# Optimization experiments

Hardware: AMD Instinct MI355X
Metric: run time of the kernel (lower is better)

Reference implementation:

```python
import jax, jax.numpy as jnp
import numpy as np

D = 512
H = 4
DK = D // H
N_ACTOR = 4096
N_BV = 4096
NEG = jnp.float32(-1e9)  # stands in for -inf; exp underflows to exactly 0 in fp32


def setup_inputs() -> dict:
    key = jax.random.key(0)
    k1, k2, k3, k4, k5, k6, k7, k8 = jax.random.split(key, 8)
    a_z = jax.random.normal(k1, (N_ACTOR, D), dtype=jnp.float32)
    bv_z = jax.random.normal(k2, (N_BV, D), dtype=jnp.float32)
    mask = jax.random.uniform(k3, (N_ACTOR, N_BV)) > 0.5
    weight = jax.random.normal(k4, (N_ACTOR, N_BV), dtype=jnp.float32)
    # nn.MultiheadAttention parameters (packed in_proj, out_proj)
    in_proj_w = jax.random.normal(k5, (3 * D, D), dtype=jnp.float32) * 0.02
    in_proj_b = jax.random.normal(k6, (3 * D,), dtype=jnp.float32) * 0.02
    out_w = jax.random.normal(k7, (D, D), dtype=jnp.float32) * 0.02
    out_b = jax.random.normal(k8, (D,), dtype=jnp.float32) * 0.02
    return {"a_z": a_z, "bv_z": bv_z, "mask": mask, "weight": weight,
            "in_proj_w": in_proj_w, "in_proj_b": in_proj_b,
            "out_w": out_w, "out_b": out_b}


def reference(a_z, bv_z, mask, weight, in_proj_w, in_proj_b, out_w, out_b):
    n, d = a_z.shape
    m = bv_z.shape[0]
    a = jnp.nan_to_num(a_z, nan=0.0, posinf=1.0, neginf=-1.0)
    kv = jnp.nan_to_num(bv_z, nan=0.0, posinf=1.0, neginf=-1.0)
    w = jnp.nan_to_num(weight, nan=0.0, posinf=1.0, neginf=-1.0)
    mf = mask.astype(a.dtype)
    valid = jnp.any(mask, axis=1)  # actors with at least one unmasked key

    # attn_mask = weight masked with -inf at padded keys (covers key_padding_mask too)
    bias = jnp.where(mask, w, NEG)  # [n, m]

    wq, wk, wv = jnp.split(in_proj_w, 3, axis=0)
    bq, bk, bv = jnp.split(in_proj_b, 3, axis=0)
    q = ((a @ wq.T + bq).reshape(n, H, DK)) * (1.0 / np.sqrt(DK))
    k = (kv @ wk.T + bk).reshape(m, H, DK)
    v = (kv @ wv.T + bv).reshape(m, H, DK)

    scores = jnp.einsum('nhd,mhd->nhm', q, k) + bias[:, None, :]
    attn = jax.nn.softmax(scores, axis=-1)                  # [n, h, m]
    ctx = jnp.einsum('nhm,mhd->nhd', attn, v).reshape(n, d)
    out = ctx @ out_w.T + out_b                              # out_proj

    # topic alignment: mean over head-chunks of the projected output
    topic = out.reshape(n, H, DK).mean(axis=1)               # [n, dk]

    # influence: softmax-normalized weight scores dotted with avg attn weights
    aw = attn.mean(axis=1) * mf                              # head-averaged attn, masked
    norm_scores = jax.nn.softmax(bias, axis=-1) * mf
    influence = jnp.sum(norm_scores * aw, axis=-1)           # [n]

    # actors with no valid key are scattered back as zeros
    topic = jnp.where(valid[:, None], topic, 0.0)
    influence = jnp.where(valid, influence, 0.0)
    return topic, influence
```

## Files before the change

kernel.cpp:

```cpp
#include <hip/hip_runtime.h>
#include <hip/hip_bf16.h>
#include <cstdint>
#include <cstddef>


typedef __attribute__((ext_vector_type(8))) short bf16x8;
typedef __attribute__((ext_vector_type(4))) short bf16x4;
typedef __attribute__((ext_vector_type(4))) float f32x4;

#define MFMA32(a, b, c) __builtin_amdgcn_mfma_f32_16x16x32_bf16((a), (b), (c), 0, 0, 0)
#define MFMA16(a, b, c) __builtin_amdgcn_mfma_f32_16x16x16bf16_1k((a), (b), (c), 0, 0, 0)

static __device__ __forceinline__ short f2b(float x) {
  union { float f; unsigned u; } v; v.f = x;
  unsigned r = v.u + 0x7fffu + ((v.u >> 16) & 1u);
  return (short)(r >> 16);
}

__global__ __launch_bounds__(256) void k_qkv(
    const float* __restrict__ a, const float* __restrict__ kv,
    const float* __restrict__ w, const float* __restrict__ bias,
    short* __restrict__ Qb, short* __restrict__ Kp, short* __restrict__ Vp)
{
  __shared__ short As[128 * 40];
  __shared__ short Bs[128 * 40];
  const int blk = blockIdx.x;
  const int bm = blk / 12, bn = blk % 12;
  const int m0 = bm * 128, n0 = bn * 128;
  const float* __restrict__ Ain = (bn < 4) ? a : kv;
  const int tid = threadIdx.x;
  const int lane = tid & 63, wv = tid >> 6;
  const int wm = (wv >> 1) * 64, wn = (wv & 1) * 64;
  const int c = lane & 15, g = lane >> 4;
  const int srow = tid >> 1, scol = (tid & 1) * 16;

  f32x4 acc[4][4];
#pragma unroll
  for (int i = 0; i < 4; ++i)
#pragma unroll
    for (int j = 0; j < 4; ++j) acc[i][j] = (f32x4)0.f;

  for (int k0 = 0; k0 < 512; k0 += 32) {
    const float* ap = Ain + (size_t)(m0 + srow) * 512 + k0 + scol;
    const float* bp = w + (size_t)(n0 + srow) * 512 + k0 + scol;
#pragma unroll
    for (int j = 0; j < 4; ++j) {
      f32x4 av = *(const f32x4*)(ap + 4 * j);
      f32x4 bv = *(const f32x4*)(bp + 4 * j);
      bf16x4 as, bs;
      as.x = f2b(av.x); as.y = f2b(av.y); as.z = f2b(av.z); as.w = f2b(av.w);
      bs.x = f2b(bv.x); bs.y = f2b(bv.y); bs.z = f2b(bv.z); bs.w = f2b(bv.w);
      *(bf16x4*)(&As[srow * 40 + scol + 4 * j]) = as;
      *(bf16x4*)(&Bs[srow * 40 + scol + 4 * j]) = bs;
    }
    __syncthreads();
    bf16x8 af[4], bfg[4];
#pragma unroll
    for (int t = 0; t < 4; ++t) {
      af[t]  = *(const bf16x8*)(&As[(wm + t * 16 + c) * 40 + g * 8]);
      bfg[t] = *(const bf16x8*)(&Bs[(wn + t * 16 + c) * 40 + g * 8]);
    }
#pragma unroll
    for (int rt = 0; rt < 4; ++rt)
#pragma unroll
      for (int ct = 0; ct < 4; ++ct)
        acc[rt][ct] = MFMA32(af[rt], bfg[ct], acc[rt][ct]);
    __syncthreads();
  }

#pragma unroll
  for (int ct = 0; ct < 4; ++ct) {
    const int col = n0 + wn + ct * 16 + c;
    const float bj = bias[col];
#pragma unroll
    for (int rt = 0; rt < 4; ++rt) {
      const int row = m0 + wm + rt * 16 + g * 4;
      const int mc = row >> 4;
      if (bn < 4) {
#pragma unroll
        for (int r = 0; r < 4; ++r)
          Qb[(size_t)(row + r) * 512 + col] = f2b((acc[rt][ct][r] + bj) * 0.08838834764831843f);
      } else if (bn < 8) {
        const int colK = col - 512;
        const int h = colK >> 7, dk = colK & 127;
        const int ks = dk >> 5, gk = (dk >> 3) & 3, j = dk & 7;
        short* base = Kp + (size_t)((((h * 256 + mc) * 4 + ks) * 64) + gk * 16 + g * 4) * 8 + j;
#pragma unroll
        for (int r = 0; r < 4; ++r) base[r * 8] = f2b(acc[rt][ct][r] + bj);
      } else {
        const int colV = col - 1024;
        const int h = colV >> 7, db = (colV & 127) >> 4, cv = colV & 15;
        bf16x4 pk;
#pragma unroll
        for (int r = 0; r < 4; ++r) pk[r] = f2b(acc[rt][ct][r] + bj);
        *(bf16x4*)(Vp + (size_t)((((h * 256 + mc) * 8 + db) * 64) + g * 16 + cv) * 4) = pk;
      }
    }
  }
}

__global__ __launch_bounds__(256, 4) void k_attn(
    const short* __restrict__ Qb, const short* __restrict__ Kp,
    const short* __restrict__ Vp, const float* __restrict__ wgt,
    const int* __restrict__ msk, const int S,
    short* __restrict__ Opart, float* __restrict__ lpart,
    float* __restrict__ cipart, float* __restrict__ lbpart)
{
  const int bx = blockIdx.x;
  const int rb = bx & 255, sp = bx >> 8;
  const int n0 = rb * 16;
  const int mlen = 4096 / S;
  const int mc0 = (sp * mlen) >> 4;
  const int nch = mlen >> 4;
  const int tid = threadIdx.x;
  const int lane = tid & 63, h = tid >> 6;
  const int c = lane & 15, g = lane >> 4;

  bf16x8 qf[4];
#pragma unroll
  for (int ks = 0; ks < 4; ++ks)
    qf[ks] = *(const bf16x8*)(Qb + (size_t)(n0 + c) * 512 + h * 128 + ks * 32 + g * 8);

  f32x4 O[8];
#pragma unroll
  for (int db = 0; db < 8; ++db) O[db] = (f32x4)0.f;
  float lh = 0.f, lb = 0.f, ci = 0.f;

  const short* Kw = Kp + (size_t)h * 524288 + (size_t)lane * 8;
  const short* Vw = Vp + (size_t)h * 524288 + (size_t)lane * 4;
  const size_t ebase = (size_t)(n0 + c) * 4096 + g * 4;

  for (int t = 0; t < nch; ++t) {
    const int mc = mc0 + t;
    const int4 mk = *(const int4*)(msk + ebase + mc * 16);
    const f32x4 wvv = *(const f32x4*)(wgt + ebase + mc * 16);
    bf16x8 kf[4];
#pragma unroll
    for (int ks = 0; ks < 4; ++ks)
      kf[ks] = *(const bf16x8*)(Kw + mc * 2048 + ks * 512);
    f32x4 Sv = (f32x4)0.f;
#pragma unroll
    for (int ks = 0; ks < 4; ++ks) Sv = MFMA32(kf[ks], qf[ks], Sv);
    const float e0 = mk.x ? __expf(wvv.x) : 0.f;
    const float e1 = mk.y ? __expf(wvv.y) : 0.f;
    const float e2 = mk.z ? __expf(wvv.z) : 0.f;
    const float e3 = mk.w ? __expf(wvv.w) : 0.f;
    const float p0 = __expf(Sv[0]) * e0, p1 = __expf(Sv[1]) * e1;
    const float p2 = __expf(Sv[2]) * e2, p3 = __expf(Sv[3]) * e3;
    lh += (p0 + p1) + (p2 + p3);
    lb += (e0 + e1) + (e2 + e3);
    ci += (p0 * e0 + p1 * e1) + (p2 * e2 + p3 * e3);
    bf16x4 pa;
    pa[0] = f2b(p0); pa[1] = f2b(p1); pa[2] = f2b(p2); pa[3] = f2b(p3);
#pragma unroll
    for (int db = 0; db < 8; ++db) {
      const bf16x4 vf = *(const bf16x4*)(Vw + mc * 2048 + db * 256);
      O[db] = MFMA16(pa, vf, O[db]);
    }
  }

  lh += __shfl_xor(lh, 16, 64); lh += __shfl_xor(lh, 32, 64);
  lb += __shfl_xor(lb, 16, 64); lb += __shfl_xor(lb, 32, 64);
  ci += __shfl_xor(ci, 16, 64); ci += __shfl_xor(ci, 32, 64);

  float inv[4];
#pragma unroll
  for (int r = 0; r < 4; ++r)
    inv[r] = 1.f / fmaxf(__shfl(lh, 4 * g + r, 64), 1e-30f);
#pragma unroll
  for (int db = 0; db < 8; ++db)
#pragma unroll
    for (int r = 0; r < 4; ++r)
      Opart[(size_t)sp * (4096 * 512) + (size_t)(n0 + g * 4 + r) * 512 +
            h * 128 + db * 16 + c] = f2b(O[db][r] * inv[r]);

  if (g == 0) {
    const int row = n0 + c;
    lpart[((size_t)sp * 4 + h) * 4096 + row] = lh;
    cipart[((size_t)sp * 4 + h) * 4096 + row] = ci;
    if (h == 0) lbpart[(size_t)sp * 4096 + row] = lb;
  }
}

__global__ __launch_bounds__(256) void k_comb(
    const short* __restrict__ Opart, const float* __restrict__ lpart,
    const float* __restrict__ cipart, const float* __restrict__ lbpart,
    const int S, short* __restrict__ ctxb, float* __restrict__ validw,
    float* __restrict__ infl)
{
  const int tid = threadIdx.x;
  const int rloc = tid >> 5, cseg = tid & 31;
  const int row = blockIdx.x * 8 + rloc;
  const int col0 = cseg * 16;
  const int h = col0 >> 7;

  float l[4], ciS[4], lb = 0.f;
#pragma unroll
  for (int hh = 0; hh < 4; ++hh) { l[hh] = 0.f; ciS[hh] = 0.f; }
  for (int s = 0; s < S; ++s) {
#pragma unroll
    for (int hh = 0; hh < 4; ++hh) {
      l[hh]   += lpart[((size_t)s * 4 + hh) * 4096 + row];
      ciS[hh] += cipart[((size_t)s * 4 + hh) * 4096 + row];
    }
    lb += lbpart[(size_t)s * 4096 + row];
  }

  float acc[16];
#pragma unroll
  for (int j = 0; j < 16; ++j) acc[j] = 0.f;
  const float linv = 1.f / fmaxf(l[h], 1e-30f);
  for (int s = 0; s < S; ++s) {
    const float w_s = lpart[((size_t)s * 4 + h) * 4096 + row] * linv;
    const bf16x8 o0 = *(const bf16x8*)(Opart + (size_t)s * (4096 * 512) + (size_t)row * 512 + col0);
    const bf16x8 o1 = *(const bf16x8*)(Opart + (size_t)s * (4096 * 512) + (size_t)row * 512 + col0 + 8);
#pragma unroll
    for (int j = 0; j < 8; ++j) {
      union { unsigned u; float f; } v0, v1;
      v0.u = ((unsigned)(unsigned short)o0[j]) << 16;
      v1.u = ((unsigned)(unsigned short)o1[j]) << 16;
      acc[j]     += w_s * v0.f;
      acc[8 + j] += w_s * v1.f;
    }
  }
  bf16x8 c0, c1;
#pragma unroll
  for (int j = 0; j < 8; ++j) { c0[j] = f2b(acc[j]); c1[j] = f2b(acc[8 + j]); }
  *(bf16x8*)(ctxb + (size_t)row * 512 + col0) = c0;
  *(bf16x8*)(ctxb + (size_t)row * 512 + col0 + 8) = c1;

  if (cseg == 0) {
    validw[row] = (lb > 0.f) ? 1.f : 0.f;
    float s_ = 0.f;
#pragma unroll
    for (int hh = 0; hh < 4; ++hh) s_ += ciS[hh] / fmaxf(l[hh], 1e-30f);
    infl[row] = (lb > 0.f) ? s_ / (4.f * lb) : 0.f;
  }
}

__global__ void k_fold(const float* __restrict__ ow, const float* __restrict__ ob,
                       short* __restrict__ Wf, float* __restrict__ bfo)
{
  const int idx = blockIdx.x * 256 + threadIdx.x;
  if (idx < 128 * 512) {
    const int dk = idx >> 9, d = idx & 511;
    const float s = 0.25f * (ow[(size_t)dk * 512 + d] + ow[(size_t)(dk + 128) * 512 + d] +
                             ow[(size_t)(dk + 256) * 512 + d] + ow[(size_t)(dk + 384) * 512 + d]);
    Wf[(size_t)dk * 512 + d] = f2b(s);
  }
  if (idx < 128) bfo[idx] = 0.25f * (ob[idx] + ob[idx + 128] + ob[idx + 256] + ob[idx + 384]);
}

__global__ __launch_bounds__(256) void k_out(
    const short* __restrict__ ctxb, const short* __restrict__ Wf,
    const float* __restrict__ bfo, const float* __restrict__ validw,
    float* __restrict__ topic)
{
  const int tid = threadIdx.x;
  const int lane = tid & 63, wv = tid >> 6;
  const int m0 = blockIdx.x * 64 + wv * 16;
  const int c = lane & 15, g = lane >> 4;

  f32x4 acc[8];
#pragma unroll
  for (int db = 0; db < 8; ++db) acc[db] = (f32x4)0.f;

  for (int k0 = 0; k0 < 512; k0 += 32) {
    const bf16x8 af = *(const bf16x8*)(ctxb + (size_t)(m0 + c) * 512 + k0 + g * 8);
#pragma unroll
    for (int db = 0; db < 8; ++db) {
      const bf16x8 bfr = *(const bf16x8*)(Wf + (size_t)(db * 16 + c) * 512 + k0 + g * 8);
      acc[db] = MFMA32(af, bfr, acc[db]);
    }
  }

#pragma unroll
  for (int r = 0; r < 4; ++r) {
    const int row = m0 + g * 4 + r;
    const float va = validw[row];
#pragma unroll
    for (int db = 0; db < 8; ++db) {
      const int col = db * 16 + c;
      const float vl = (va > 0.5f) ? (acc[db][r] + bfo[col]) : 0.f;
      topic[(size_t)row * 128 + col] = vl;
    }
  }
}

extern "C" void kernel_launch(void* const* d_in, const int* in_sizes, int n_in,
                              void* d_out, int out_size, void* d_ws, size_t ws_size,
                              hipStream_t stream) {
  const float* a_z  = (const float*)d_in[0];
  const float* bv_z = (const float*)d_in[1];
  const int*   mask = (const int*)d_in[2];
  const float* wgt  = (const float*)d_in[3];
  const float* ipw  = (const float*)d_in[4];
  const float* ipb  = (const float*)d_in[5];
  const float* ow   = (const float*)d_in[6];
  const float* ob   = (const float*)d_in[7];
  float* topic = (float*)d_out;
  float* infl  = (float*)d_out + 4096 * 128;

  const size_t MB = (size_t)1 << 20;
  char* ws = (char*)d_ws;
  short* Qb     = (short*)(ws);
  short* Kp     = (short*)(ws + 4 * MB);
  short* Vp     = (short*)(ws + 8 * MB);
  short* ctxb   = (short*)(ws + 12 * MB);
  float* validw = (float*)(ws + 16 * MB);
  short* Wf     = (short*)(ws + 16 * MB + (64 << 10));
  float* bfo    = (float*)(ws + 16 * MB + (224 << 10));
  const size_t pbase0 = 16 * MB + (256 << 10);

  auto need = [&](int S) { return pbase0 + (size_t)S * (4 * MB + (144 << 10)); };
  int S = 4;
  while (S > 1 && need(S) > ws_size) S >>= 1;

  char* pbase = ws + pbase0;
  short* Opart  = (short*)(pbase);
  float* lpart  = (float*)(pbase + (size_t)S * 4 * MB);
  float* cipart = (float*)(pbase + (size_t)S * 4 * MB + ((size_t)S << 16));
  float* lbpart = (float*)(pbase + (size_t)S * 4 * MB + ((size_t)S << 17));

  k_qkv <<<384, 256, 0, stream>>>(a_z, bv_z, ipw, ipb, Qb, Kp, Vp);
  k_fold<<<256, 256, 0, stream>>>(ow, ob, Wf, bfo);
  k_attn<<<256 * S, 256, 0, stream>>>(Qb, Kp, Vp, wgt, mask, S, Opart, lpart, cipart, lbpart);
  k_comb<<<512, 256, 0, stream>>>(Opart, lpart, cipart, lbpart, S, ctxb, validw, infl);
  k_out <<<64, 256, 0, stream>>>(ctxb, Wf, bfo, validw, topic);
}
```

Measured before the change: 377.1 us.

## Shrink GEMM tiles, prefetch mask/weight, raise KV split and out-proj grid

The QKV GEMM tile goes from 128x128 to 128x64, doubling the grid to 768 blocks. The out-proj kernel now has each wave compute 32 columns of a 16-row tile, across 256 blocks. Together these put more blocks on the device's CUs. The attention kernel software-prefetches mask and weight two chunks ahead, and the key split S rises from 4 to 8 when workspace allows, adding parallelism at the cost of more partial-output traffic in the combine kernel. Smaller tiles reduce operand reuse and increase redundant loads of A and W.

```diff
diff --git a/kernel.cpp b/kernel.cpp
--- a/kernel.cpp
+++ b/kernel.cpp
@@ -23,64 +23,70 @@
     short* __restrict__ Qb, short* __restrict__ Kp, short* __restrict__ Vp)
 {
   __shared__ short As[128 * 40];
-  __shared__ short Bs[128 * 40];
+  __shared__ short Bs[64 * 40];
   const int blk = blockIdx.x;
-  const int bm = blk / 12, bn = blk % 12;
-  const int m0 = bm * 128, n0 = bn * 128;
-  const float* __restrict__ Ain = (bn < 4) ? a : kv;
+  const int bm = blk % 32, bn = blk / 32;
+  const int m0 = bm * 128, n0 = bn * 64;
+  const float* __restrict__ Ain = (bn < 8) ? a : kv;
   const int tid = threadIdx.x;
-  const int lane = tid & 63, wv = tid >> 6;
-  const int wm = (wv >> 1) * 64, wn = (wv & 1) * 64;
+  const int lane = tid & 63, wvi = tid >> 6;
+  const int wm = (wvi >> 1) * 64, wn = (wvi & 1) * 32;
   const int c = lane & 15, g = lane >> 4;
-  const int srow = tid >> 1, scol = (tid & 1) * 16;
-
-  f32x4 acc[4][4];
+  const int srA = tid >> 1, scA = (tid & 1) * 16;
+  const int srB = tid >> 2, scB = (tid & 3) * 8;
+
+  f32x4 acc[4][2];
 #pragma unroll
   for (int i = 0; i < 4; ++i)
 #pragma unroll
-    for (int j = 0; j < 4; ++j) acc[i][j] = (f32x4)0.f;
+    for (int j = 0; j < 2; ++j) acc[i][j] = (f32x4)0.f;
 
   for (int k0 = 0; k0 < 512; k0 += 32) {
-    const float* ap = Ain + (size_t)(m0 + srow) * 512 + k0 + scol;
-    const float* bp = w + (size_t)(n0 + srow) * 512 + k0 + scol;
+    const float* ap = Ain + (size_t)(m0 + srA) * 512 + k0 + scA;
 #pragma unroll
     for (int j = 0; j < 4; ++j) {
       f32x4 av = *(const f32x4*)(ap + 4 * j);
+      bf16x4 as;
+      as.x = f2b(av.x); as.y = f2b(av.y); as.z = f2b(av.z); as.w = f2b(av.w);
+      *(bf16x4*)(&As[srA * 40 + scA + 4 * j]) = as;
+    }
+    const float* bp = w + (size_t)(n0 + srB) * 512 + k0 + scB;
+#pragma unroll
+    for (int j = 0; j < 2; ++j) {
       f32x4 bv = *(const f32x4*)(bp + 4 * j);
-      bf16x4 as, bs;
-      as.x = f2b(av.x); as.y = f2b(av.y); as.z = f2b(av.z); as.w = f2b(av.w);
+      bf16x4 bs;
       bs.x = f2b(bv.x); bs.y = f2b(bv.y); bs.z = f2b(bv.z); bs.w = f2b(bv.w);
-      *(bf16x4*)(&As[srow * 40 + scol + 4 * j]) = as;
-      *(bf16x4*)(&Bs[srow * 40 + scol + 4 * j]) = bs;
+      *(bf16x4*)(&Bs[srB * 40 + scB + 4 * j]) = bs;
     }
     __syncthreads();
-    bf16x8 af[4], bfg[4];
-#pragma unroll
-    for (int t = 0; t < 4; ++t) {
-      af[t]  = *(const bf16x8*)(&As[(wm + t * 16 + c) * 40 + g * 8]);
+    bf16x8 af[4], bfg[2];
+#pragma unroll
+    for (int t = 0; t < 4; ++t)
+      af[t] = *(const bf16x8*)(&As[(wm + t * 16 + c) * 40 + g * 8]);
+#pragma unroll
+    for (int t = 0; t < 2; ++t)
       bfg[t] = *(const bf16x8*)(&Bs[(wn + t * 16 + c) * 40 + g * 8]);
-    }
 #pragma unroll
     for (int rt = 0; rt < 4; ++rt)
 #pragma unroll
-      for (int ct = 0; ct < 4; ++ct)
+      for (int ct = 0; ct < 2; ++ct)
         acc[rt][ct] = MFMA32(af[rt], bfg[ct], acc[rt][ct]);
     __syncthreads();
   }
 
 #pragma unroll
-  for (int ct = 0; ct < 4; ++ct) {
+  for (int ct = 0; ct < 2; ++ct) {
     const int col = n0 + wn + ct * 16 + c;
     const float bj = bias[col];
 #pragma unroll
     for (int rt = 0; rt < 4; ++rt) {
       const int row = m0 + wm + rt * 16 + g * 4;
       const int mc = row >> 4;
-      if (bn < 4) {
+      if (col < 512) {
 #pragma unroll
         for (int r = 0; r < 4; ++r)
           Qb[(size_t)(row + r) * 512 + col] = f2b((acc[rt][ct][r] + bj) * 0.08838834764831843f);
-      } else if (bn < 8) {
+      } else if (col < 1024) {
         const int colK = col - 512;
         const int h = colK >> 7, dk = colK & 127;
         const int ks = dk >> 5, gk = (dk >> 3) & 3, j = dk & 7;
@@ -126,25 +132,23 @@
   for (int db = 0; db < 8; ++db) O[db] = (f32x4)0.f;
   float lh = 0.f, lb = 0.f, ci = 0.f;
 
-  const short* Kw = Kp + (size_t)h * 524288 + (size_t)lane * 8;
-  const short* Vw = Vp + (size_t)h * 524288 + (size_t)lane * 4;
-  const size_t ebase = (size_t)(n0 + c) * 4096 + g * 4;
-
-  for (int t = 0; t < nch; ++t) {
-    const int mc = mc0 + t;
-    const int4 mk = *(const int4*)(msk + ebase + mc * 16);
-    const f32x4 wvv = *(const f32x4*)(wgt + ebase + mc * 16);
+  const short* Kw = Kp + (size_t)h * 524288 + (size_t)lane * 8 + (size_t)mc0 * 2048;
+  const short* Vw = Vp + (size_t)h * 524288 + (size_t)lane * 4 + (size_t)mc0 * 2048;
+  const int* mbase_p = msk + (size_t)(n0 + c) * 4096 + g * 4 + (size_t)mc0 * 16;
+  const float* wbase_p = wgt + (size_t)(n0 + c) * 4096 + g * 4 + (size_t)mc0 * 16;
+
+  auto chunk = [&](int t, const int4& mk, const f32x4& wv) {
     bf16x8 kf[4];
 #pragma unroll
     for (int ks = 0; ks < 4; ++ks)
-      kf[ks] = *(const bf16x8*)(Kw + mc * 2048 + ks * 512);
+      kf[ks] = *(const bf16x8*)(Kw + t * 2048 + ks * 512);
     f32x4 Sv = (f32x4)0.f;
 #pragma unroll
     for (int ks = 0; ks < 4; ++ks) Sv = MFMA32(kf[ks], qf[ks], Sv);
-    const float e0 = mk.x ? __expf(wvv.x) : 0.f;
-    const float e1 = mk.y ? __expf(wvv.y) : 0.f;
-    const float e2 = mk.z ? __expf(wvv.z) : 0.f;
-    const float e3 = mk.w ? __expf(wvv.w) : 0.f;
+    const float e0 = mk.x ? __expf(wv.x) : 0.f;
+    const float e1 = mk.y ? __expf(wv.y) : 0.f;
+    const float e2 = mk.z ? __expf(wv.z) : 0.f;
+    const float e3 = mk.w ? __expf(wv.w) : 0.f;
     const float p0 = __expf(Sv[0]) * e0, p1 = __expf(Sv[1]) * e1;
     const float p2 = __expf(Sv[2]) * e2, p3 = __expf(Sv[3]) * e3;
     lh += (p0 + p1) + (p2 + p3);
@@ -154,9 +158,24 @@
     pa[0] = f2b(p0); pa[1] = f2b(p1); pa[2] = f2b(p2); pa[3] = f2b(p3);
 #pragma unroll
     for (int db = 0; db < 8; ++db) {
-      const bf16x4 vf = *(const bf16x4*)(Vw + mc * 2048 + db * 256);
+      const bf16x4 vf = *(const bf16x4*)(Vw + t * 2048 + db * 256);
       O[db] = MFMA16(pa, vf, O[db]);
     }
+  };
+
+  int4 mkA = *(const int4*)(mbase_p);
+  f32x4 wvA = *(const f32x4*)(wbase_p);
+  int4 mkB = *(const int4*)(mbase_p + 16);
+  f32x4 wvB = *(const f32x4*)(wbase_p + 16);
+
+  for (int t = 0; t < nch; t += 2) {
+    int4 mkC = mkA, mkD = mkB;
+    f32x4 wvC = wvA, wvD = wvB;
+    if (t + 2 < nch) { mkC = *(const int4*)(mbase_p + (t + 2) * 16); wvC = *(const f32x4*)(wbase_p + (t + 2) * 16); }
+    if (t + 3 < nch) { mkD = *(const int4*)(mbase_p + (t + 3) * 16); wvD = *(const f32x4*)(wbase_p + (t + 3) * 16); }
+    chunk(t, mkA, wvA);
+    chunk(t + 1, mkB, wvB);
+    mkA = mkC; wvA = wvC; mkB = mkD; wvB = wvD;
   }
 
   lh += __shfl_xor(lh, 16, 64); lh += __shfl_xor(lh, 32, 64);
@@ -257,20 +276,19 @@
     float* __restrict__ topic)
 {
   const int tid = threadIdx.x;
-  const int lane = tid & 63, wv = tid >> 6;
-  const int m0 = blockIdx.x * 64 + wv * 16;
+  const int lane = tid & 63, wvi = tid >> 6;
+  const int m0 = blockIdx.x * 16;
   const int c = lane & 15, g = lane >> 4;
 
-  f32x4 acc[8];
-#pragma unroll
-  for (int db = 0; db < 8; ++db) acc[db] = (f32x4)0.f;
+  f32x4 acc[2];
+  acc[0] = (f32x4)0.f; acc[1] = (f32x4)0.f;
 
   for (int k0 = 0; k0 < 512; k0 += 32) {
     const bf16x8 af = *(const bf16x8*)(ctxb + (size_t)(m0 + c) * 512 + k0 + g * 8);
 #pragma unroll
-    for (int db = 0; db < 8; ++db) {
-      const bf16x8 bfr = *(const bf16x8*)(Wf + (size_t)(db * 16 + c) * 512 + k0 + g * 8);
-      acc[db] = MFMA32(af, bfr, acc[db]);
+    for (int dbl = 0; dbl < 2; ++dbl) {
+      const bf16x8 bfr = *(const bf16x8*)(Wf + (size_t)(wvi * 32 + dbl * 16 + c) * 512 + k0 + g * 8);
+      acc[dbl] = MFMA32(af, bfr, acc[dbl]);
     }
   }
 
@@ -279,9 +297,9 @@
     const int row = m0 + g * 4 + r;
     const float va = validw[row];
 #pragma unroll
-    for (int db = 0; db < 8; ++db) {
-      const int col = db * 16 + c;
-      const float vl = (va > 0.5f) ? (acc[db][r] + bfo[col]) : 0.f;
+    for (int dbl = 0; dbl < 2; ++dbl) {
+      const int col = wvi * 32 + dbl * 16 + c;
+      const float vl = (va > 0.5f) ? (acc[dbl][r] + bfo[col]) : 0.f;
       topic[(size_t)row * 128 + col] = vl;
     }
   }
@@ -313,7 +331,7 @@
   const size_t pbase0 = 16 * MB + (256 << 10);
 
   auto need = [&](int S) { return pbase0 + (size_t)S * (4 * MB + (144 << 10)); };
-  int S = 4;
+  int S = 8;
   while (S > 1 && need(S) > ws_size) S >>= 1;
 
   char* pbase = ws + pbase0;
@@ -322,9 +340,9 @@
   float* cipart = (float*)(pbase + (size_t)S * 4 * MB + ((size_t)S << 16));
   float* lbpart = (float*)(pbase + (size_t)S * 4 * MB + ((size_t)S << 17));
 
-  k_qkv <<<384, 256, 0, stream>>>(a_z, bv_z, ipw, ipb, Qb, Kp, Vp);
+  k_qkv <<<768, 256, 0, stream>>>(a_z, bv_z, ipw, ipb, Qb, Kp, Vp);
   k_fold<<<256, 256, 0, stream>>>(ow, ob, Wf, bfo);
   k_attn<<<256 * S, 256, 0, stream>>>(Qb, Kp, Vp, wgt, mask, S, Opart, lpart, cipart, lbpart);
   k_comb<<<512, 256, 0, stream>>>(Opart, lpart, cipart, lbpart, S, ctxb, validw, infl);
-  k_out <<<64, 256, 0, stream>>>(ctxb, Wf, bfo, validw, topic);
-}
+  k_out <<<256, 256, 0, stream>>>(ctxb, Wf, bfo, validw, topic);
+}
```

Result: slower. 500.0 us (+32.6%).
